# Kernel optimization log

Measured on AMD Instinct MI355X. Metric: run time of the kernel, lower is better.

## Reference

```python
import itertools
import jax, jax.numpy as jnp
import numpy as np

N_NODES = 100000
N_EDGES = 1600000
D = 32
C = 16
PDIM = 2  # pseudo-coordinate dim (SplineConv dim=E)


def setup_inputs() -> dict:
    key = jax.random.key(0)
    ks = jax.random.split(key, 16)
    s = 0.1
    inp = {
        "x": jax.random.normal(ks[0], (N_NODES, D), jnp.float32),
        "edge_index": jax.random.randint(ks[1], (2, N_EDGES), 0, N_NODES, jnp.int32),
        "edge_attr": jax.random.uniform(ks[2], (N_EDGES, PDIM), jnp.float32),
        # SplineConv 1: kernel_size=3 per dim -> K1 = 3**PDIM weight matrices
        "W1": jax.random.normal(ks[3], (3 ** PDIM, D, D), jnp.float32) * s,
        "root1": jax.random.normal(ks[4], (D, D), jnp.float32) * s,
        "bias1": jax.random.normal(ks[5], (D,), jnp.float32) * s,
        # SplineConv 2: kernel_size=5 per dim -> K2 = 5**PDIM weight matrices
        "W2": jax.random.normal(ks[6], (5 ** PDIM, D, D), jnp.float32) * s,
        "root2": jax.random.normal(ks[7], (D, D), jnp.float32) * s,
        "bias2": jax.random.normal(ks[8], (D,), jnp.float32) * s,
        "mlp1_w": jax.random.normal(ks[9], (D, D), jnp.float32) * s,
        "mlp1_b": jax.random.normal(ks[10], (D,), jnp.float32) * s,
        "mlp2_w": jax.random.normal(ks[11], (D, C), jnp.float32) * s,
        "mlp2_b": jax.random.normal(ks[12], (C,), jnp.float32) * s,
    }
    return inp


def _spline_conv(x, src, dst, pseudo, W, root, bias, ksize):
    """SplineConv, degree-1 open B-splines, aggr='mean' (torch_geometric default)."""
    N, d = x.shape
    dim = pseudo.shape[1]
    K = ksize ** dim
    E = src.shape[0]
    v = pseudo * (ksize - 1)          # [E, dim] in [0, ksize-1]
    bot = jnp.floor(v)
    frac = v - bot                    # linear B-spline fractional weight
    boti = bot.astype(jnp.int32)
    # Precompute per-kernel transformed features: y[n,k,:] = x[n] @ W[k]
    y = jnp.einsum('nd,kde->nke', x, W).reshape(N * K, d)
    msg = jnp.zeros((E, d), x.dtype)
    # (degree+1)^dim = 2^dim spline taps per edge; fixed small loop
    for offs in itertools.product((0, 1), repeat=dim):
        b = jnp.ones((E,), x.dtype)
        kidx = jnp.zeros((E,), jnp.int32)
        stride = 1
        for dd in range(dim):
            b = b * (frac[:, dd] if offs[dd] else (1.0 - frac[:, dd]))
            kidx = kidx + jnp.minimum(boti[:, dd] + offs[dd], ksize - 1) * stride
            stride *= ksize
        msg = msg + b[:, None] * y[src * K + kidx]
    agg = jax.ops.segment_sum(msg, dst, num_segments=N)
    cnt = jax.ops.segment_sum(jnp.ones((E,), x.dtype), dst, num_segments=N)
    cnt = jnp.clip(cnt, 1.0, None)
    return agg / cnt[:, None] + x @ root + bias


def reference(x, edge_index, edge_attr, W1, root1, bias1, W2, root2, bias2,
              mlp1_w, mlp1_b, mlp2_w, mlp2_b):
    src, dst = edge_index[0], edge_index[1]
    h = jax.nn.elu(_spline_conv(x, src, dst, edge_attr, W1, root1, bias1, 3))
    # dropout is identity at inference (F.dropout with training=False)
    h = jax.nn.elu(_spline_conv(h, src, dst, edge_attr, W2, root2, bias2, 5))
    h = jax.nn.relu(h @ mlp1_w + mlp1_b)
    h = jax.nn.relu(h @ mlp2_w + mlp2_b)
    return h
```

## Files before the change

### kernel.cpp

```cpp
#include <hip/hip_runtime.h>
#include <math.h>

#define NN 100000
#define NE 1600000
#define DD 32
#define CC 16

typedef unsigned short bf16_t;
typedef __attribute__((ext_vector_type(8))) short short8v;
typedef __attribute__((ext_vector_type(4))) float float4v;

static inline unsigned gblocks(long total) { return (unsigned)((total + 255) / 256); }

__device__ inline bf16_t f2bf(float f) {
    unsigned u = __float_as_uint(f);
    u += 0x7fffu + ((u >> 16) & 1u);
    return (bf16_t)(u >> 16);
}
__device__ inline float bf2f(bf16_t h) { return __uint_as_float(((unsigned)h) << 16); }
__device__ inline unsigned pk2(float a, float b) {
    return (unsigned)f2bf(a) | ((unsigned)f2bf(b) << 16);
}

__global__ void zero_k(float* p, long n) {
    long i = (long)blockIdx.x * 256 + threadIdx.x;
    if (i < n) p[i] = 0.f;
}

__global__ void count_k(const int* __restrict__ dst, float* __restrict__ cnt) {
    int e = blockIdx.x * 256 + threadIdx.x;
    if (e < NE) atomicAdd(&cnt[dst[e]], 1.0f);
}

__global__ void castx_k(const float* __restrict__ in, bf16_t* __restrict__ outf) {
    int tid = blockIdx.x * 256 + threadIdx.x;
    if (tid >= NN * 4) return;
    int n = tid >> 2, q = tid & 3;
    const float4* ip = (const float4*)(in + (long)n * DD + q * 8);
    float4 v0 = ip[0], v1 = ip[1];
    int tile = n >> 4;
    int lane = (n & 15) + 16 * q;
    unsigned* op = (unsigned*)(outf + ((long)tile * 64 + lane) * 8);
    op[0] = pk2(v0.x, v0.y);
    op[1] = pk2(v0.z, v0.w);
    op[2] = pk2(v1.x, v1.y);
    op[3] = pk2(v1.z, v1.w);
}

__global__ void castw_k(const float* __restrict__ W, bf16_t* __restrict__ wtf, int K) {
    int tid = blockIdx.x * 256 + threadIdx.x;
    if (tid >= K * 2 * 64) return;
    int l = tid & 63;
    int half = (tid >> 6) & 1;
    int k = tid >> 7;
    int e = (l & 15) + 16 * half;
    int dbase = (l >> 4) * 8;
    bf16_t* op = wtf + (long)tid * 8;
#pragma unroll
    for (int r = 0; r < 8; ++r)
        op[r] = f2bf(W[(long)k * 1024 + (dbase + r) * DD + e]);
}

template<int K>
__global__ __launch_bounds__(64) void ymm_k(const short8v* __restrict__ xtf,
                                            const short8v* __restrict__ wtf,
                                            unsigned* __restrict__ y) {
    constexpr int RS = K * 16 + 4;
    __shared__ unsigned lds[16 * RS];
    const int l = threadIdx.x;
    const int tile = blockIdx.x;
    const int node = l & 15, g = l >> 4;

    short8v b = xtf[(long)tile * 64 + l];
    float4v zz = {0.f, 0.f, 0.f, 0.f};

    for (int k = 0; k < K; ++k) {
        float4v d0 = __builtin_amdgcn_mfma_f32_16x16x32_bf16(wtf[(2 * k + 0) * 64 + l], b, zz, 0, 0, 0);
        float4v d1 = __builtin_amdgcn_mfma_f32_16x16x32_bf16(wtf[(2 * k + 1) * 64 + l], b, zz, 0, 0, 0);
        unsigned* lr = &lds[node * RS + k * 16];
        lr[2 * g]     = pk2(d0[0], d0[1]);
        lr[2 * g + 1] = pk2(d0[2], d0[3]);
        lr[8 + 2 * g]     = pk2(d1[0], d1[1]);
        lr[8 + 2 * g + 1] = pk2(d1[2], d1[3]);
    }
    __syncthreads();

    unsigned* yb = y + (long)tile * (16 * K * 16);
    constexpr int TOT = 16 * K * 16;
    for (int off = l * 4; off < TOT; off += 256) {
        int nd = off / (K * 16);
        int rem = off - nd * (K * 16);
        const unsigned* lp = &lds[nd * RS + rem];
        uint4 v = make_uint4(lp[0], lp[1], lp[2], lp[3]);
        *(uint4*)(yb + off) = v;
    }
}

template<int KS>
__global__ void edge_y_k(const int* __restrict__ src, const int* __restrict__ dst,
                         const float* __restrict__ attr, const bf16_t* __restrict__ y,
                         float* __restrict__ agg) {
    long tid = (long)blockIdx.x * 256 + threadIdx.x;
    if (tid >= (long)NE * DD) return;
    int e = (int)(tid & (DD - 1));
    int ed = (int)(tid >> 5);
    const int K = KS * KS;
    float u0 = attr[2 * ed], u1 = attr[2 * ed + 1];
    float v0 = u0 * (KS - 1), v1 = u1 * (KS - 1);
    float fb0 = floorf(v0), fb1 = floorf(v1);
    float f0 = v0 - fb0, f1 = v1 - fb1;
    int i0 = min((int)fb0, KS - 1), i1 = min((int)fb1, KS - 1);
    int j0 = min(i0 + 1, KS - 1), j1 = min(i1 + 1, KS - 1);
    int s = src[ed];
    long base = (long)s * (K * DD) + e;
    float y00 = bf2f(y[base + (i0 + i1 * KS) * DD]);
    float y10 = bf2f(y[base + (j0 + i1 * KS) * DD]);
    float y01 = bf2f(y[base + (i0 + j1 * KS) * DD]);
    float y11 = bf2f(y[base + (j0 + j1 * KS) * DD]);
    float m = (1.f - f0) * (1.f - f1) * y00 + f0 * (1.f - f1) * y10
            + (1.f - f0) * f1 * y01 + f0 * f1 * y11;
    atomicAdd(&agg[(long)dst[ed] * DD + e], m);
}

__global__ __launch_bounds__(256) void fin_k(
        const float* __restrict__ agg, const float* __restrict__ cnt,
        const float* __restrict__ xin, const float* __restrict__ root,
        const float* __restrict__ bias, float* __restrict__ h) {
    const int lane = threadIdx.x & 31;
    const int grp = threadIdx.x >> 5;
    const int n = blockIdx.x * 8 + grp;
    if (n >= NN) return;
    float c = cnt[n]; if (c < 1.f) c = 1.f;
    float xv = xin[(long)n * DD + lane];
    float racc = 0.f;
#pragma unroll
    for (int d = 0; d < DD; ++d)
        racc = fmaf(__shfl(xv, d, 32), root[d * DD + lane], racc);
    float v = agg[(long)n * DD + lane] / c + racc + bias[lane];
    h[(long)n * DD + lane] = v > 0.f ? v : expm1f(v);
}

__global__ __launch_bounds__(256) void mlp_k(
        const float* __restrict__ h, const float* __restrict__ w1,
        const float* __restrict__ b1, const float* __restrict__ w2,
        const float* __restrict__ b2, float* __restrict__ out) {
    const int lane = threadIdx.x & 31;
    const int grp = threadIdx.x >> 5;
    const int n = blockIdx.x * 8 + grp;
    if (n >= NN) return;
    float hv = h[(long)n * DD + lane];
    float t = b1[lane];
#pragma unroll
    for (int d = 0; d < DD; ++d)
        t = fmaf(__shfl(hv, d, 32), w1[d * DD + lane], t);
    t = fmaxf(t, 0.f);
    int c = lane & (CC - 1);
    float o = 0.f;
#pragma unroll
    for (int d = 0; d < DD; ++d)
        o = fmaf(__shfl(t, d, 32), w2[d * CC + c], o);
    o += b2[c];
    o = fmaxf(o, 0.f);
    if (lane < CC) out[(long)n * CC + lane] = o;
}

extern "C" void kernel_launch(void* const* d_in, const int* in_sizes, int n_in,
                              void* d_out, int out_size, void* d_ws, size_t ws_size,
                              hipStream_t stream) {
    const float* x     = (const float*)d_in[0];
    const int*   ei    = (const int*)d_in[1];
    const float* attr  = (const float*)d_in[2];
    const float* W1    = (const float*)d_in[3];
    const float* root1 = (const float*)d_in[4];
    const float* bias1 = (const float*)d_in[5];
    const float* W2    = (const float*)d_in[6];
    const float* root2 = (const float*)d_in[7];
    const float* bias2 = (const float*)d_in[8];
    const float* m1w   = (const float*)d_in[9];
    const float* m1b   = (const float*)d_in[10];
    const float* m2w   = (const float*)d_in[11];
    const float* m2b   = (const float*)d_in[12];
    float* out = (float*)d_out;

    const int* srcp = ei;
    const int* dstp = ei + NE;

    float* cnt  = (float*)d_ws;
    float* agg  = cnt + NN;
    float* h1   = agg + (size_t)NN * DD;
    bf16_t* xtf = (bf16_t*)(h1 + (size_t)NN * DD);
    bf16_t* wtf1 = xtf + (size_t)NN * DD;
    bf16_t* wtf2 = wtf1 + 9 * 2 * 64 * 8;
    bf16_t* y   = wtf2 + 25 * 2 * 64 * 8;
    float* h2   = (float*)y;

    const unsigned gn = (NN + 7) / 8;
    const unsigned gt = NN / 16;

    zero_k<<<gblocks(NN + (long)NN * DD), 256, 0, stream>>>(cnt, NN + (long)NN * DD);
    count_k<<<gblocks(NE), 256, 0, stream>>>(dstp, cnt);

    castx_k<<<gblocks(NN * 4), 256, 0, stream>>>(x, xtf);
    castw_k<<<gblocks(9 * 2 * 64), 256, 0, stream>>>(W1, wtf1, 9);
    castw_k<<<gblocks(25 * 2 * 64), 256, 0, stream>>>(W2, wtf2, 25);

    ymm_k<9><<<gt, 64, 0, stream>>>((const short8v*)xtf, (const short8v*)wtf1, (unsigned*)y);
    edge_y_k<3><<<gblocks((long)NE * DD), 256, 0, stream>>>(srcp, dstp, attr, y, agg);
    fin_k<<<gn, 256, 0, stream>>>(agg, cnt, x, root1, bias1, h1);

    castx_k<<<gblocks(NN * 4), 256, 0, stream>>>(h1, xtf);
    zero_k<<<gblocks((long)NN * DD), 256, 0, stream>>>(agg, (long)NN * DD);
    ymm_k<25><<<gt, 64, 0, stream>>>((const short8v*)xtf, (const short8v*)wtf2, (unsigned*)y);
    edge_y_k<5><<<gblocks((long)NE * DD), 256, 0, stream>>>(srcp, dstp, attr, y, agg);
    fin_k<<<gn, 256, 0, stream>>>(agg, cnt, h1, root2, bias2, h2);

    mlp_k<<<gn, 256, 0, stream>>>(h2, m1w, m1b, m2w, m2b, out);
}
```

Measured before the change: 622.1 us.

## Sort edges by destination via counting sort to localize scatter atomics

Builds a destination-sorted edge permutation with a histogram, a three-pass prefix scan and an atomic fill. The edge kernels then walk edges in that order, so atomics hitting the same aggregate row come from adjacent threads, which should improve locality and coalescing of the scatter-adds. Node degrees now come from the CSR offsets, and workspace buffers are reused in place. The cost is several extra preprocessing launches plus an indirection through perm that scatters the src and attr reads.

```diff
diff --git a/kernel.cpp b/kernel.cpp
--- a/kernel.cpp
+++ b/kernel.cpp
@@ -5,6 +5,7 @@
 #define NE 1600000
 #define DD 32
 #define CC 16
+#define SCAN_B 391
 
 typedef unsigned short bf16_t;
 typedef __attribute__((ext_vector_type(8))) short short8v;
@@ -27,9 +28,68 @@
     if (i < n) p[i] = 0.f;
 }
 
-__global__ void count_k(const int* __restrict__ dst, float* __restrict__ cnt) {
+__global__ void zero_int_k(int* p, int n) {
+    int i = blockIdx.x * 256 + threadIdx.x;
+    if (i < n) p[i] = 0;
+}
+
+__global__ void hist_k(const int* __restrict__ dst, int* __restrict__ cnt) {
     int e = blockIdx.x * 256 + threadIdx.x;
-    if (e < NE) atomicAdd(&cnt[dst[e]], 1.0f);
+    if (e < NE) atomicAdd(&cnt[dst[e]], 1);
+}
+
+__global__ void s1_k(const int* __restrict__ cnt, int* __restrict__ offs,
+                     int* __restrict__ bsum) {
+    __shared__ int sm[256];
+    int t = threadIdx.x, b = blockIdx.x;
+    int g = b * 256 + t;
+    int v = (g < NN) ? cnt[g] : 0;
+    sm[t] = v;
+    __syncthreads();
+    for (int o = 1; o < 256; o <<= 1) {
+        int u = (t >= o) ? sm[t - o] : 0;
+        __syncthreads();
+        sm[t] += u;
+        __syncthreads();
+    }
+    if (g < NN) offs[g + 1] = sm[t];
+    if (t == 255) bsum[b] = sm[255];
+}
+
+__global__ void s2_k(int* __restrict__ bsum) {
+    __shared__ int sm[512];
+    int t = threadIdx.x;
+    int v = (t < SCAN_B) ? bsum[t] : 0;
+    sm[t] = v;
+    __syncthreads();
+    for (int o = 1; o < 512; o <<= 1) {
+        int u = (t >= o) ? sm[t - o] : 0;
+        __syncthreads();
+        sm[t] += u;
+        __syncthreads();
+    }
+    if (t < SCAN_B) bsum[t] = sm[t] - v;
+}
+
+__global__ void s3_k(int* __restrict__ offs, const int* __restrict__ bsum) {
+    int t = threadIdx.x, b = blockIdx.x;
+    int g = b * 256 + t;
+    if (g < NN) offs[g + 1] += bsum[b];
+    if (g == 0) offs[0] = 0;
+}
+
+__global__ void copyoff_k(const int* __restrict__ offs, int* __restrict__ cur) {
+    int g = blockIdx.x * 256 + threadIdx.x;
+    if (g < NN) cur[g] = offs[g];
+}
+
+__global__ void fill_k(const int* __restrict__ dst, int* __restrict__ cur,
+                       int* __restrict__ perm) {
+    int e = blockIdx.x * 256 + threadIdx.x;
+    if (e < NE) {
+        int pos = atomicAdd(&cur[dst[e]], 1);
+        perm[pos] = e;
+    }
 }
 
 __global__ void castx_k(const float* __restrict__ in, bf16_t* __restrict__ outf) {
@@ -97,21 +157,23 @@
 }
 
 template<int KS>
-__global__ void edge_y_k(const int* __restrict__ src, const int* __restrict__ dst,
-                         const float* __restrict__ attr, const bf16_t* __restrict__ y,
-                         float* __restrict__ agg) {
+__global__ void edge_s_k(const int* __restrict__ perm, const int* __restrict__ src,
+                         const int* __restrict__ dst, const float2* __restrict__ attr,
+                         const bf16_t* __restrict__ y, float* __restrict__ agg) {
     long tid = (long)blockIdx.x * 256 + threadIdx.x;
     if (tid >= (long)NE * DD) return;
     int e = (int)(tid & (DD - 1));
-    int ed = (int)(tid >> 5);
+    int j = (int)(tid >> 5);
+    int ed = perm[j];
     const int K = KS * KS;
-    float u0 = attr[2 * ed], u1 = attr[2 * ed + 1];
-    float v0 = u0 * (KS - 1), v1 = u1 * (KS - 1);
+    float2 uv = attr[ed];
+    int s = src[ed];
+    int dn = dst[ed];
+    float v0 = uv.x * (KS - 1), v1 = uv.y * (KS - 1);
     float fb0 = floorf(v0), fb1 = floorf(v1);
     float f0 = v0 - fb0, f1 = v1 - fb1;
     int i0 = min((int)fb0, KS - 1), i1 = min((int)fb1, KS - 1);
     int j0 = min(i0 + 1, KS - 1), j1 = min(i1 + 1, KS - 1);
-    int s = src[ed];
     long base = (long)s * (K * DD) + e;
     float y00 = bf2f(y[base + (i0 + i1 * KS) * DD]);
     float y10 = bf2f(y[base + (j0 + i1 * KS) * DD]);
@@ -119,25 +181,26 @@
     float y11 = bf2f(y[base + (j0 + j1 * KS) * DD]);
     float m = (1.f - f0) * (1.f - f1) * y00 + f0 * (1.f - f1) * y10
             + (1.f - f0) * f1 * y01 + f0 * f1 * y11;
-    atomicAdd(&agg[(long)dst[ed] * DD + e], m);
+    atomicAdd(&agg[(long)dn * DD + e], m);
 }
 
 __global__ __launch_bounds__(256) void fin_k(
-        const float* __restrict__ agg, const float* __restrict__ cnt,
+        float* __restrict__ agg, const int* __restrict__ offs,
         const float* __restrict__ xin, const float* __restrict__ root,
-        const float* __restrict__ bias, float* __restrict__ h) {
+        const float* __restrict__ bias) {
     const int lane = threadIdx.x & 31;
     const int grp = threadIdx.x >> 5;
     const int n = blockIdx.x * 8 + grp;
     if (n >= NN) return;
-    float c = cnt[n]; if (c < 1.f) c = 1.f;
+    int deg = offs[n + 1] - offs[n];
+    float c = deg > 0 ? (float)deg : 1.f;
     float xv = xin[(long)n * DD + lane];
     float racc = 0.f;
 #pragma unroll
     for (int d = 0; d < DD; ++d)
         racc = fmaf(__shfl(xv, d, 32), root[d * DD + lane], racc);
     float v = agg[(long)n * DD + lane] / c + racc + bias[lane];
-    h[(long)n * DD + lane] = v > 0.f ? v : expm1f(v);
+    agg[(long)n * DD + lane] = v > 0.f ? v : expm1f(v);
 }
 
 __global__ __launch_bounds__(256) void mlp_k(
@@ -185,34 +248,43 @@
     const int* srcp = ei;
     const int* dstp = ei + NE;
 
-    float* cnt  = (float*)d_ws;
-    float* agg  = cnt + NN;
-    float* h1   = agg + (size_t)NN * DD;
-    bf16_t* xtf = (bf16_t*)(h1 + (size_t)NN * DD);
-    bf16_t* wtf1 = xtf + (size_t)NN * DD;
+    int* offs = (int*)d_ws;
+    int* perm = offs + NN + 8;
+    float* aggA = (float*)(perm + NE);
+    float* aggB = aggA + (size_t)NN * DD;
+    bf16_t* wtf1 = (bf16_t*)(aggB + (size_t)NN * DD);
     bf16_t* wtf2 = wtf1 + 9 * 2 * 64 * 8;
-    bf16_t* y   = wtf2 + 25 * 2 * 64 * 8;
-    float* h2   = (float*)y;
+    bf16_t* y = wtf2 + 25 * 2 * 64 * 8;
+
+    int* cur  = (int*)aggA;
+    int* bsum = (int*)aggA + NN;
+    bf16_t* xtf = (bf16_t*)aggB;
 
     const unsigned gn = (NN + 7) / 8;
     const unsigned gt = NN / 16;
 
-    zero_k<<<gblocks(NN + (long)NN * DD), 256, 0, stream>>>(cnt, NN + (long)NN * DD);
-    count_k<<<gblocks(NE), 256, 0, stream>>>(dstp, cnt);
-
-    castx_k<<<gblocks(NN * 4), 256, 0, stream>>>(x, xtf);
+    zero_int_k<<<gblocks(NN), 256, 0, stream>>>(cur, NN);
+    hist_k<<<gblocks(NE), 256, 0, stream>>>(dstp, cur);
+    s1_k<<<SCAN_B, 256, 0, stream>>>(cur, offs, bsum);
+    s2_k<<<1, 512, 0, stream>>>(bsum);
+    s3_k<<<SCAN_B, 256, 0, stream>>>(offs, bsum);
+    copyoff_k<<<SCAN_B, 256, 0, stream>>>(offs, cur);
+    fill_k<<<gblocks(NE), 256, 0, stream>>>(dstp, cur, perm);
+
     castw_k<<<gblocks(9 * 2 * 64), 256, 0, stream>>>(W1, wtf1, 9);
     castw_k<<<gblocks(25 * 2 * 64), 256, 0, stream>>>(W2, wtf2, 25);
 
+    castx_k<<<gblocks(NN * 4), 256, 0, stream>>>(x, xtf);
     ymm_k<9><<<gt, 64, 0, stream>>>((const short8v*)xtf, (const short8v*)wtf1, (unsigned*)y);
-    edge_y_k<3><<<gblocks((long)NE * DD), 256, 0, stream>>>(srcp, dstp, attr, y, agg);
-    fin_k<<<gn, 256, 0, stream>>>(agg, cnt, x, root1, bias1, h1);
-
-    castx_k<<<gblocks(NN * 4), 256, 0, stream>>>(h1, xtf);
-    zero_k<<<gblocks((long)NN * DD), 256, 0, stream>>>(agg, (long)NN * DD);
+    zero_k<<<gblocks((long)NN * DD), 256, 0, stream>>>(aggA, (long)NN * DD);
+    edge_s_k<3><<<gblocks((long)NE * DD), 256, 0, stream>>>(perm, srcp, dstp, (const float2*)attr, y, aggA);
+    fin_k<<<gn, 256, 0, stream>>>(aggA, offs, x, root1, bias1);
+
+    castx_k<<<gblocks(NN * 4), 256, 0, stream>>>(aggA, xtf);
     ymm_k<25><<<gt, 64, 0, stream>>>((const short8v*)xtf, (const short8v*)wtf2, (unsigned*)y);
-    edge_y_k<5><<<gblocks((long)NE * DD), 256, 0, stream>>>(srcp, dstp, attr, y, agg);
-    fin_k<<<gn, 256, 0, stream>>>(agg, cnt, h1, root2, bias2, h2);
-
-    mlp_k<<<gn, 256, 0, stream>>>(h2, m1w, m1b, m2w, m2b, out);
-}
+    zero_k<<<gblocks((long)NN * DD), 256, 0, stream>>>(aggB, (long)NN * DD);
+    edge_s_k<5><<<gblocks((long)NE * DD), 256, 0, stream>>>(perm, srcp, dstp, (const float2*)attr, y, aggB);
+    fin_k<<<gn, 256, 0, stream>>>(aggB, offs, aggA, root2, bias2);
+
+    mlp_k<<<gn, 256, 0, stream>>>(aggB, m1w, m1b, m2w, m2b, out);
+}
```

New measurement: 1.373 ms. +120.8%, slower.
